# Kernel optimization log

Measured on AMD Instinct MI355X. Metric: run time of the kernel, lower is better.

Reference implementation:

```python
import jax, jax.numpy as jnp
import numpy as np

B, N_VIS, N_HID1, N_HID2 = 1024, 4096, 4096, 4096


def setup_inputs() -> dict:
    key = jax.random.key(0)
    k0, k1, k2, k3 = jax.random.split(key, 4)
    v_data = (jax.random.uniform(k0, (B, N_VIS)) < 0.5).astype(jnp.float32)
    occupant_data = (jax.random.uniform(k1, (B, N_VIS // 2)) < 0.5).astype(jnp.float32)
    bw1 = float(np.sqrt(6.0 / (N_HID1 + N_VIS)))   # xavier_uniform
    bw2 = float(np.sqrt(6.0 / (N_HID1 + N_HID2)))
    W1 = jax.random.uniform(k2, (N_HID1, N_VIS), jnp.float32, -bw1, bw1)
    W2 = jax.random.uniform(k3, (N_HID1, N_HID2), jnp.float32, -bw2, bw2)
    return {
        "v_data": v_data,
        "occupant_data": occupant_data,
        "W1": W1,
        "b_v": jnp.zeros((N_VIS,), jnp.float32),
        "b_h1": jnp.zeros((N_HID1,), jnp.float32),
        "W2": W2,
        "b_h2": jnp.zeros((N_HID2,), jnp.float32),
        "k": 2,
    }


def reference(v_data, occupant_data, W1, b_v, b_h1, W2, b_h2, k):
    key = jax.random.key(42)
    Bn, n_vis = v_data.shape
    n_hid2 = b_h2.shape[0]
    dt = v_data.dtype

    def bern(kk, p):
        return (jax.random.uniform(kk, p.shape, p.dtype) < p).astype(p.dtype)

    # literal torch math (n_hid1 == n_hid2):
    # F.linear(v, W1, b_h1) + F.linear(h2, W2.T) = v@W1.T + b_h1 + h2@W2
    def p_h1(v, h2):
        return jax.nn.sigmoid(v @ W1.T + b_h1 + h2 @ W2)

    def p_h2(h1):  # F.linear(h1, W2, b_h2) = h1@W2.T + b_h2
        return jax.nn.sigmoid(h1 @ W2.T + b_h2)

    def p_v(h1):   # F.linear(h1, W1.T, b_v) = h1@W1 + b_v
        return jax.nn.sigmoid(h1 @ W1 + b_v)

    kpos1, kpos2, kfin, kloop = jax.random.split(key, 4)

    # positive phase (no_grad in torch)
    h2_zeros = jnp.zeros((Bn, n_hid2), dt)
    h1_data = bern(kpos1, jax.lax.stop_gradient(p_h1(v_data, h2_zeros)))
    h2_data = bern(kpos2, jax.lax.stop_gradient(p_h2(h1_data)))

    # negative phase: k Gibbs steps with occupant clamping
    v_neg, h2_neg = v_data, h2_data
    for i in range(k):
        ka, kb, kc = jax.random.split(jax.random.fold_in(kloop, i), 3)
        h1_neg = bern(ka, p_h1(v_neg, h2_neg))
        h2_neg = bern(kb, p_h2(h1_neg))
        pv = p_v(h1_neg)
        sign_s = bern(kc, pv[:, 1::2])
        # occupant_clamp: occupant bits from data, sign bits sampled
        v_neg = jnp.stack([occupant_data, sign_s], axis=-1).reshape(Bn, n_vis)

    h1_neg_final = bern(kfin, jax.lax.stop_gradient(p_h1(v_neg, h2_neg)))

    pos_v_sign = v_data[:, 1::2]
    neg_v_sign = v_neg[:, 1::2]
    invB = 1.0 / Bn

    # mean over batch of outer products == single matmul / B
    dW1_sign = (jnp.einsum('bi,bj->ij', pos_v_sign, h1_data)
                - jnp.einsum('bi,bj->ij', neg_v_sign, h1_neg_final)) * invB
    dW1_full = jnp.zeros_like(W1).at[:, 1::2].set(dW1_sign.T)
    db_v_full = jnp.zeros_like(b_v).at[1::2].set((pos_v_sign - neg_v_sign).mean(0))
    db_h1 = (h1_data - h1_neg_final).mean(0)
    dW2 = (jnp.einsum('bi,bj->ij', h1_data, h2_data)
           - jnp.einsum('bi,bj->ij', h1_neg_final, h2_neg)) * invB
    db_h2 = (h2_data - h2_neg).mean(0)

    eps = jnp.asarray(1e-7, dt)
    sp, st = v_neg[:, 1::2], v_data[:, 1::2]
    loss = -(st * jnp.log(sp + eps) + (1 - st) * jnp.log(1 - sp + eps)).mean()

    # torch sets p.grad = -dX; return loss plus those grads
    return (loss, -dW1_full, -db_v_full, -db_h1, -dW2, -db_h2)
```

## Files before the change

kernel.cpp:

```cpp
#include <hip/hip_runtime.h>
#include <stdint.h>
#include <math.h>

#define B_SZ 1024
#define NV   4096
#define NH   4096
#define NSGN 2048

typedef short bf16x8 __attribute__((ext_vector_type(8)));
typedef short bf16x4 __attribute__((ext_vector_type(4)));
typedef float f32x4  __attribute__((ext_vector_type(4)));
typedef _Float16 f16x8 __attribute__((ext_vector_type(8)));

#define F16_ONE  ((short)0x3C00)
#define F16_NEG1 ((short)0xBC00)

__device__ __forceinline__ short f32_to_f16s(float f)
{
    union { _Float16 h; short s; } u;
    u.h = (_Float16)f;
    return u.s;
}

__host__ __device__ __forceinline__ void tf2x32(uint32_t k0, uint32_t k1,
                                                uint32_t x0, uint32_t x1,
                                                uint32_t& o0, uint32_t& o1)
{
    uint32_t k2 = k0 ^ k1 ^ 0x1BD11BDAu;
#define TFR(r) { x0 += x1; x1 = (x1 << (r)) | (x1 >> (32 - (r))); x1 ^= x0; }
    x0 += k0; x1 += k1;
    TFR(13) TFR(15) TFR(26) TFR(6)
    x0 += k1; x1 += k2 + 1u;
    TFR(17) TFR(29) TFR(16) TFR(24)
    x0 += k2; x1 += k0 + 2u;
    TFR(13) TFR(15) TFR(26) TFR(6)
    x0 += k0; x1 += k1 + 3u;
    TFR(17) TFR(29) TFR(16) TFR(24)
    x0 += k1; x1 += k2 + 4u;
    TFR(13) TFR(15) TFR(26) TFR(6)
    x0 += k2; x1 += k0 + 5u;
#undef TFR
    o0 = x0; o1 = x1;
}

__device__ __forceinline__ float tf_uniform01(uint32_t k0, uint32_t k1, uint32_t idx)
{
    uint32_t a, b;
    tf2x32(k0, k1, 0u, idx, a, b);
    uint32_t bits = a ^ b;
    uint32_t fb = (bits >> 9) | 0x3F800000u;
    return __uint_as_float(fb) - 1.0f;
}

__device__ __forceinline__ float sigmoidf_(float x)
{
    if (x >= 0.0f) { float e = expf(-x); return 1.0f / (1.0f + e); }
    float e = expf(x); return e / (1.0f + e);
}

__device__ __forceinline__ void gl16(const void* g, void* l)
{
    __builtin_amdgcn_global_load_lds((const __attribute__((address_space(1))) void*)g,
                                     (__attribute__((address_space(3))) void*)l, 16, 0, 0);
}

__global__ __launch_bounds__(256) void conv_tr(const float* __restrict__ W,
                                               short* __restrict__ Wf,
                                               short* __restrict__ Wt)
{
    __shared__ short t[64][65];
    const int bx = blockIdx.x * 64;
    const int by = blockIdx.y * 64;
    const int r0 = threadIdx.x >> 4;
    const int c0 = (threadIdx.x & 15) * 4;
#pragma unroll
    for (int i = 0; i < 4; ++i) {
        int row = by + r0 + i * 16;
        f32x4 v = *(const f32x4*)(W + (size_t)row * 4096 + bx + c0);
        short h[4];
#pragma unroll
        for (int j = 0; j < 4; ++j) h[j] = f32_to_f16s(v[j]);
        *(bf16x4*)(Wf + (size_t)row * 4096 + bx + c0) = *(bf16x4*)h;
#pragma unroll
        for (int j = 0; j < 4; ++j) t[c0 + j][r0 + i * 16] = h[j];
    }
    __syncthreads();
#pragma unroll
    for (int i = 0; i < 4; ++i) {
        int orow = r0 + i * 16;
        short o[4] = { t[orow][c0], t[orow][c0 + 1], t[orow][c0 + 2], t[orow][c0 + 3] };
        *(bf16x4*)(Wt + (size_t)(bx + orow) * 4096 + by + c0) = *(bf16x4*)o;
    }
}

__global__ __launch_bounds__(256) void conv_f16(const float* __restrict__ W,
                                                short* __restrict__ Wf)
{
    size_t i = ((size_t)blockIdx.x * 256 + threadIdx.x) * 4;
    f32x4 v = *(const f32x4*)(W + i);
    short h[4];
#pragma unroll
    for (int c = 0; c < 4; ++c) h[c] = f32_to_f16s(v[c]);
    *(bf16x4*)(Wf + i) = *(bf16x4*)h;
}

__global__ __launch_bounds__(256) void conv_trodd(const float* __restrict__ W,
                                                  short* __restrict__ Wt)
{
    __shared__ short t[64][65];
    const int bx = blockIdx.x * 64;
    const int by = blockIdx.y * 64;
    const int r0 = threadIdx.x >> 4;
    const int c0 = (threadIdx.x & 15) * 4;
#pragma unroll
    for (int i = 0; i < 4; ++i) {
        int row = by + r0 + i * 16;
        const float* p = W + (size_t)row * 4096 + 2 * (bx + c0);
        f32x4 a = *(const f32x4*)p;
        f32x4 b = *(const f32x4*)(p + 4);
        t[c0 + 0][r0 + i * 16] = f32_to_f16s(a[1]);
        t[c0 + 1][r0 + i * 16] = f32_to_f16s(a[3]);
        t[c0 + 2][r0 + i * 16] = f32_to_f16s(b[1]);
        t[c0 + 3][r0 + i * 16] = f32_to_f16s(b[3]);
    }
    __syncthreads();
#pragma unroll
    for (int i = 0; i < 4; ++i) {
        int orow = r0 + i * 16;
        short o[4] = { t[orow][c0], t[orow][c0 + 1], t[orow][c0 + 2], t[orow][c0 + 3] };
        *(bf16x4*)(Wt + (size_t)(bx + orow) * 4096 + by + c0) = *(bf16x4*)o;
    }
}

template<int NEG>
__global__ __launch_bounds__(256) void tr16(const short* __restrict__ in,
                                            short* __restrict__ out)
{
    __shared__ short t[64][65];
    const int bx = blockIdx.x * 64;
    const int by = blockIdx.y * 64;
    const int r0 = threadIdx.x >> 4;
    const int c0 = (threadIdx.x & 15) * 4;
#pragma unroll
    for (int i = 0; i < 4; ++i) {
        int row = by + r0 + i * 16;
        bf16x4 v = *(const bf16x4*)(in + (size_t)row * 4096 + bx + c0);
#pragma unroll
        for (int j = 0; j < 4; ++j)
            t[c0 + j][r0 + i * 16] = NEG ? (short)(v[j] ^ (short)0x8000) : v[j];
    }
    __syncthreads();
#pragma unroll
    for (int i = 0; i < 4; ++i) {
        int orow = r0 + i * 16;
        short o[4] = { t[orow][c0], t[orow][c0 + 1], t[orow][c0 + 2], t[orow][c0 + 3] };
        *(bf16x4*)(out + (size_t)(bx + orow) * 1024 + by + c0) = *(bf16x4*)o;
    }
}

__global__ __launch_bounds__(256) void tr_sign(const short* __restrict__ in,
                                               short* __restrict__ out)
{
    __shared__ short t[64][65];
    const int bx = blockIdx.x * 64;
    const int by = blockIdx.y * 64;
    const int r0 = threadIdx.x >> 4;
    const int c0 = (threadIdx.x & 15) * 4;
#pragma unroll
    for (int i = 0; i < 4; ++i) {
        int row = by + r0 + i * 16;
        bf16x8 v = *(const bf16x8*)(in + (size_t)row * 4096 + 2 * (bx + c0));
#pragma unroll
        for (int j = 0; j < 4; ++j) t[c0 + j][r0 + i * 16] = v[2 * j + 1];
    }
    __syncthreads();
#pragma unroll
    for (int i = 0; i < 4; ++i) {
        int orow = r0 + i * 16;
        short o[4] = { t[orow][c0], t[orow][c0 + 1], t[orow][c0 + 2], t[orow][c0 + 3] };
        *(bf16x4*)(out + (size_t)(bx + orow) * 1024 + by + c0) = *(bf16x4*)o;
    }
}

__global__ __launch_bounds__(256) void tr_signf(const float* __restrict__ in,
                                                short* __restrict__ out)
{
    __shared__ short t[64][65];
    const int bx = blockIdx.x * 64;
    const int by = blockIdx.y * 64;
    const int r0 = threadIdx.x >> 4;
    const int c0 = (threadIdx.x & 15) * 4;
#pragma unroll
    for (int i = 0; i < 4; ++i) {
        int row = by + r0 + i * 16;
        const float* p = in + (size_t)row * 4096 + 2 * (bx + c0);
        f32x4 a = *(const f32x4*)p;
        f32x4 b = *(const f32x4*)(p + 4);
        t[c0 + 0][r0 + i * 16] = (a[1] != 0.0f) ? F16_NEG1 : (short)0;
        t[c0 + 1][r0 + i * 16] = (a[3] != 0.0f) ? F16_NEG1 : (short)0;
        t[c0 + 2][r0 + i * 16] = (b[1] != 0.0f) ? F16_NEG1 : (short)0;
        t[c0 + 3][r0 + i * 16] = (b[3] != 0.0f) ? F16_NEG1 : (short)0;
    }
    __syncthreads();
#pragma unroll
    for (int i = 0; i < 4; ++i) {
        int orow = r0 + i * 16;
        short o[4] = { t[orow][c0], t[orow][c0 + 1], t[orow][c0 + 2], t[orow][c0 + 3] };
        *(bf16x4*)(out + (size_t)(bx + orow) * 1024 + by + c0) = *(bf16x4*)o;
    }
}

template<int MODE>
__global__ __launch_bounds__(512, 2) void mm_chunk(
    const short* __restrict__ A0, const short* __restrict__ A1,
    const short* __restrict__ B0, const short* __restrict__ B1,
    short* __restrict__ P)
{
    __shared__ __align__(1024) short As[2][16 * 512];
    __shared__ __align__(1024) short Bs[2][8 * 512];

    const int bid = blockIdx.x;
    const int xcd = bid & 7, slot = bid >> 3;

    int bm, bncol, ck, kbase, NW;
    const short* Ap;
    const short* Bp;
    if (MODE == 2) {
        int slot6 = slot % 6, rest = slot / 6;
        int pn = xcd * 6 + slot6;
        bm = (rest & 3) * 256;
        ck = rest >> 2;
        kbase = ck * 2048;
        Ap = A0;
        Bp = (pn < 32) ? (B0 + (size_t)pn * 128 * 4096)
                       : (B1 + (size_t)(pn - 32) * 128 * 4096);
        bncol = pn * 128;
        NW = 6144;
    } else {
        int pn = xcd * 4 + (slot & 3);
        bm = ((slot >> 2) & 3) * 256;
        ck = slot >> 4;
        if (MODE == 1) {
            if (ck >= 2) { Ap = A1; Bp = B1 + (size_t)pn * 128 * 4096; kbase = (ck - 2) * 2048; }
            else         { Ap = A0; Bp = B0 + (size_t)pn * 128 * 4096; kbase = ck * 2048; }
        } else {
            Ap = A0; Bp = B0 + (size_t)pn * 128 * 4096; kbase = ck * 1024;
        }
        bncol = pn * 128;
        NW = 4096;
    }

    const int NT = (MODE == 0) ? 32 : 64;

    const int tid = threadIdx.x;
    const int wv = tid >> 6, lane = tid & 63;
    const int l15 = lane & 15, l4 = lane >> 4;
    const int fr = l15, fc = l4 * 8;
    const int wm = wv >> 1, wn = wv & 1;

    f32x4 acc[4][4] = {};

    auto stage = [&](int buf, int t) {
        const int kk = kbase + t * 32;
        gl16(Ap + (size_t)(bm + (wv * 2 + 0) * 16 + fr) * 4096 + kk + fc, &As[buf][(wv * 2 + 0) * 512]);
        gl16(Ap + (size_t)(bm + (wv * 2 + 1) * 16 + fr) * 4096 + kk + fc, &As[buf][(wv * 2 + 1) * 512]);
        gl16(Bp + (size_t)(wv * 16 + fr) * 4096 + kk + fc, &Bs[buf][wv * 512]);
    };
    auto compute = [&](int buf) {
        f16x8 xf[4], yf[4];
#pragma unroll
        for (int m = 0; m < 4; ++m)
            xf[m] = *(f16x8*)&As[buf][(wm * 4 + m) * 512 + lane * 8];
#pragma unroll
        for (int n = 0; n < 4; ++n)
            yf[n] = *(f16x8*)&Bs[buf][(wn * 4 + n) * 512 + lane * 8];
#pragma unroll
        for (int m = 0; m < 4; ++m)
#pragma unroll
            for (int n = 0; n < 4; ++n)
                acc[m][n] = __builtin_amdgcn_mfma_f32_16x16x32_f16(xf[m], yf[n], acc[m][n], 0, 0, 0);
    };

    stage(0, 0);
    __syncthreads();
    for (int t = 0; t < NT; ++t) {
        const int cur = t & 1;
        if (t + 1 < NT) stage(cur ^ 1, t + 1);
        compute(cur);
        __syncthreads();
    }

    short* Pc = P + (size_t)ck * 1024 * NW;
#pragma unroll
    for (int m = 0; m < 4; ++m)
#pragma unroll
        for (int n = 0; n < 4; ++n)
#pragma unroll
            for (int r = 0; r < 4; ++r) {
                int row = bm + wm * 64 + m * 16 + l4 * 4 + r;
                int col = bncol + wn * 64 + n * 16 + l15;
                Pc[(size_t)row * NW + col] = f32_to_f16s(acc[m][n][r]);
            }
}

__global__ __launch_bounds__(512, 2) void grad2(
    const short* __restrict__ XnT, const short* __restrict__ YnT,
    const short* __restrict__ XpT, const short* __restrict__ YpT,
    float* __restrict__ Out)
{
    __shared__ __align__(1024) short As[2][16 * 512];
    __shared__ __align__(1024) short Bs[2][8 * 512];

    const int bid = blockIdx.x;
    const int xcd = bid & 7, slot = bid >> 3;
    const int pn = xcd * 4 + (slot & 3);
    const int bm = (slot >> 2) * 256;

    const int tid = threadIdx.x;
    const int wv = tid >> 6, lane = tid & 63;
    const int l15 = lane & 15, l4 = lane >> 4;
    const int fr = l15, fc = l4 * 8;
    const int wm = wv >> 1, wn = wv & 1;

    f32x4 acc[4][4] = {};

    auto stage = [&](int buf, int t) {
        const short* X = (t < 32) ? XnT : XpT;
        const short* Y = (t < 32) ? YnT : YpT;
        const int kk = (t & 31) * 32;
        gl16(X + (size_t)(bm + (wv * 2 + 0) * 16 + fr) * 1024 + kk + fc, &As[buf][(wv * 2 + 0) * 512]);
        gl16(X + (size_t)(bm + (wv * 2 + 1) * 16 + fr) * 1024 + kk + fc, &As[buf][(wv * 2 + 1) * 512]);
        gl16(Y + (size_t)(pn * 128 + wv * 16 + fr) * 1024 + kk + fc, &Bs[buf][wv * 512]);
    };
    auto compute = [&](int buf) {
        f16x8 xf[4], yf[4];
#pragma unroll
        for (int m = 0; m < 4; ++m)
            xf[m] = *(f16x8*)&As[buf][(wm * 4 + m) * 512 + lane * 8];
#pragma unroll
        for (int n = 0; n < 4; ++n)
            yf[n] = *(f16x8*)&Bs[buf][(wn * 4 + n) * 512 + lane * 8];
#pragma unroll
        for (int m = 0; m < 4; ++m)
#pragma unroll
            for (int n = 0; n < 4; ++n)
                acc[m][n] = __builtin_amdgcn_mfma_f32_16x16x32_f16(xf[m], yf[n], acc[m][n], 0, 0, 0);
    };

    stage(0, 0);
    __syncthreads();
    for (int t = 0; t < 64; ++t) {
        const int cur = t & 1;
        if (t + 1 < 64) stage(cur ^ 1, t + 1);
        compute(cur);
        __syncthreads();
    }

    const float invB = 1.0f / 1024.0f;
#pragma unroll
    for (int m = 0; m < 4; ++m)
#pragma unroll
        for (int n = 0; n < 4; ++n)
#pragma unroll
            for (int r = 0; r < 4; ++r) {
                int i_ = bm + wm * 64 + m * 16 + l4 * 4 + r;
                int j_ = pn * 128 + wn * 64 + n * 16 + l15;
                Out[(size_t)i_ * 4096 + j_] = acc[m][n][r] * invB;
            }
}

__global__ __launch_bounds__(256, 4) void grad1(
    const short* __restrict__ XnT, const short* __restrict__ YnT,
    const short* __restrict__ XpT, const short* __restrict__ YpT,
    float* __restrict__ Out)
{
    __shared__ __align__(1024) short As[2][8 * 512];
    __shared__ __align__(1024) short Bs[2][8 * 512];

    const int bid = blockIdx.x;
    const int xcd = bid & 7, slot = bid >> 3;
    const int pn = xcd * 2 + (slot & 1);
    const int bm = (slot >> 1) * 128;

    const int tid = threadIdx.x;
    const int wv = tid >> 6, lane = tid & 63;
    const int l15 = lane & 15, l4 = lane >> 4;
    const int fr = l15, fc = l4 * 8;
    const int wm = wv >> 1, wn = wv & 1;

    f32x4 acc[4][4] = {};

    auto stage = [&](int buf, int t) {
        const short* X = (t < 32) ? XnT : XpT;
        const short* Y = (t < 32) ? YnT : YpT;
        const int kk = (t & 31) * 32;
#pragma unroll
        for (int c = 0; c < 2; ++c) {
            int sub = wv * 2 + c;
            gl16(X + (size_t)(bm + sub * 16 + fr) * 1024 + kk + fc, &As[buf][sub * 512]);
            gl16(Y + (size_t)(pn * 128 + sub * 16 + fr) * 1024 + kk + fc, &Bs[buf][sub * 512]);
        }
    };
    auto compute = [&](int buf) {
        f16x8 xf[4], yf[4];
#pragma unroll
        for (int m = 0; m < 4; ++m)
            xf[m] = *(f16x8*)&As[buf][(wm * 4 + m) * 512 + lane * 8];
#pragma unroll
        for (int n = 0; n < 4; ++n)
            yf[n] = *(f16x8*)&Bs[buf][(wn * 4 + n) * 512 + lane * 8];
#pragma unroll
        for (int m = 0; m < 4; ++m)
#pragma unroll
            for (int n = 0; n < 4; ++n)
                acc[m][n] = __builtin_amdgcn_mfma_f32_16x16x32_f16(xf[m], yf[n], acc[m][n], 0, 0, 0);
    };

    stage(0, 0);
    __syncthreads();
    for (int t = 0; t < 64; ++t) {
        const int cur = t & 1;
        if (t + 1 < 64) stage(cur ^ 1, t + 1);
        compute(cur);
        __syncthreads();
    }

    const float invB = 1.0f / 1024.0f;
#pragma unroll
    for (int m = 0; m < 4; ++m)
#pragma unroll
        for (int n = 0; n < 4; ++n)
#pragma unroll
            for (int r = 0; r < 4; ++r) {
                int i_ = bm + wm * 64 + m * 16 + l4 * 4 + r;
                int j_ = pn * 128 + wn * 64 + n * 16 + l15;
                Out[(size_t)i_ * 4096 + 2 * j_ + 1] = acc[m][n][r] * invB;
                Out[(size_t)i_ * 4096 + 2 * j_]     = 0.0f;
            }
}

template<int EPI, int NC>
__global__ __launch_bounds__(256) void combine_h(
    const short* __restrict__ P, const float* __restrict__ bias,
    short* __restrict__ O0, short* __restrict__ O1,
    uint32_t k0, uint32_t k1)
{
    size_t e0 = ((size_t)blockIdx.x * 256 + threadIdx.x) * 8;
    float s[8] = {};
#pragma unroll
    for (int c = 0; c < NC; ++c) {
        f16x8 v = *(const f16x8*)(P + (size_t)c * 4194304 + e0);
#pragma unroll
        for (int j = 0; j < 8; ++j) s[j] += (float)v[j];
    }
    int col = (int)(e0 & 4095);
    short o[8];
#pragma unroll
    for (int j = 0; j < 8; ++j) {
        float v = s[j] + bias[col + j];
        float pr = sigmoidf_(v);
        float u = tf_uniform01(k0, k1, (uint32_t)(e0 + j));
        o[j] = (u < pr) ? F16_ONE : (short)0;
    }
    *(bf16x8*)&O0[e0] = *(bf16x8*)o;
    if (EPI == 1) *(bf16x8*)&O1[e0] = *(bf16x8*)o;
}

__global__ __launch_bounds__(256) void combine_dual(
    const short* __restrict__ P,
    const float* __restrict__ b_h2, const float* __restrict__ b_v,
    const float* __restrict__ occ,
    short* __restrict__ h2n, short* __restrict__ vneg,
    uint32_t kb0, uint32_t kb1, uint32_t kc0, uint32_t kc1)
{
    int idx = blockIdx.x * 256 + threadIdx.x;
    int row = idx / 768;
    int cl  = (idx - row * 768) * 8;
    float s[8] = {};
#pragma unroll
    for (int c = 0; c < 2; ++c) {
        f16x8 v = *(const f16x8*)(P + (size_t)c * 6291456 + (size_t)row * 6144 + cl);
#pragma unroll
        for (int j = 0; j < 8; ++j) s[j] += (float)v[j];
    }
    if (cl < 4096) {
        short o[8];
#pragma unroll
        for (int j = 0; j < 8; ++j) {
            float v = s[j] + b_h2[cl + j];
            float pr = sigmoidf_(v);
            size_t e = (size_t)row * 4096 + cl + j;
            float u = tf_uniform01(kb0, kb1, (uint32_t)e);
            o[j] = (u < pr) ? F16_ONE : (short)0;
        }
        *(bf16x8*)&h2n[(size_t)row * 4096 + cl] = *(bf16x8*)o;
    } else {
        int s0 = cl - 4096;
        short o[16];
#pragma unroll
        for (int j = 0; j < 8; ++j) {
            int si = s0 + j;
            float v = s[j] + b_v[2 * si + 1];
            float pr = sigmoidf_(v);
            float u = tf_uniform01(kc0, kc1, (uint32_t)(row * 2048 + si));
            o[2 * j]     = (occ[(size_t)row * 2048 + si] != 0.0f) ? F16_ONE : (short)0;
            o[2 * j + 1] = (u < pr) ? F16_ONE : (short)0;
        }
        *(bf16x8*)&vneg[(size_t)row * 4096 + 2 * s0]     = *(bf16x8*)&o[0];
        *(bf16x8*)&vneg[(size_t)row * 4096 + 2 * s0 + 8] = *(bf16x8*)&o[8];
    }
}

__global__ void cvt_kernel(const float* __restrict__ in, short* __restrict__ out, int n)
{
    int e = blockIdx.x * 256 + threadIdx.x;
    if (e < n) out[e] = (in[e] != 0.0f) ? F16_ONE : (short)0;
}

__global__ void dbv_fast(const float* __restrict__ vdata, const short* __restrict__ vneg,
                         float* __restrict__ out)
{
    __shared__ float part[4][64];
    int c = threadIdx.x & 63, rg = threadIdx.x >> 6;
    int s = blockIdx.x * 64 + c;
    float acc = 0.0f;
    for (int b = rg; b < B_SZ; b += 4)
        acc += ((vneg[(size_t)b * NV + 2 * s + 1] != 0) ? 1.0f : 0.0f)
             - vdata[(size_t)b * NV + 2 * s + 1];
    part[rg][c] = acc;
    __syncthreads();
    if (rg == 0) {
        out[2 * s + 1] = (part[0][c] + part[1][c] + part[2][c] + part[3][c]) * (1.0f / 1024.0f);
        out[2 * s] = 0.0f;
    }
}

__global__ void dbh_fast(const short* __restrict__ Xp, const short* __restrict__ Xn,
                         float* __restrict__ out)
{
    __shared__ int part[4][64];
    int c = threadIdx.x & 63, rg = threadIdx.x >> 6;
    int j = blockIdx.x * 64 + c;
    int acc = 0;
    for (int b = rg; b < B_SZ; b += 4)
        acc += (int)(Xn[(size_t)b * NH + j] != 0) - (int)(Xp[(size_t)b * NH + j] != 0);
    part[rg][c] = acc;
    __syncthreads();
    if (rg == 0)
        out[j] = (float)(part[0][c] + part[1][c] + part[2][c] + part[3][c]) * (1.0f / 1024.0f);
}

__global__ void zero_kernel(unsigned* p) { *p = 0u; }

__global__ void loss_count2(const float* __restrict__ vdata,
                            const short* __restrict__ vneg, unsigned* cnt)
{
    __shared__ int part[4];
    int t = blockIdx.x * 256 + threadIdx.x;
    int local = 0;
#pragma unroll
    for (int it = 0; it < 8; ++it) {
        int e = t + it * 262144;
        int b = e >> 11, s = e & 2047;
        float st = vdata[(size_t)b * NV + 2 * s + 1];
        float sp = (vneg[(size_t)b * NV + 2 * s + 1] != 0) ? 1.0f : 0.0f;
        local += (st != sp) ? 1 : 0;
    }
#pragma unroll
    for (int off = 32; off; off >>= 1) local += __shfl_down(local, off, 64);
    if ((threadIdx.x & 63) == 0) part[threadIdx.x >> 6] = local;
    __syncthreads();
    if (threadIdx.x == 0)
        atomicAdd(cnt, (unsigned)(part[0] + part[1] + part[2] + part[3]));
}

__global__ void loss_final_kernel(const unsigned* cnt, float* out, float lp, float lm)
{
    float mis = (float)(*cnt);
    float mat = 2097152.0f - mis;
    out[0] = -((mat * lp + mis * lm) * (1.0f / 2097152.0f));
}

extern "C" void kernel_launch(void* const* d_in, const int* in_sizes, int n_in,
                              void* d_out, int out_size, void* d_ws, size_t ws_size,
                              hipStream_t stream)
{
    (void)in_sizes; (void)n_in; (void)out_size; (void)ws_size;
    const float* v_data = (const float*)d_in[0];
    const float* occ    = (const float*)d_in[1];
    const float* W1     = (const float*)d_in[2];
    const float* b_v    = (const float*)d_in[3];
    const float* b_h1   = (const float*)d_in[4];
    const float* W2     = (const float*)d_in[5];
    const float* b_h2   = (const float*)d_in[6];
    float* out = (float*)d_out;

    char* w = (char*)d_ws;
    short* vneg = (short*)w;
    short* h1d  = vneg + (size_t)B_SZ * NV;
    short* h2d  = h1d  + (size_t)B_SZ * NH;
    short* h1c  = h2d  + (size_t)B_SZ * NH;
    short* h2n  = h1c  + (size_t)B_SZ * NH;
    short* P    = h2n + (size_t)B_SZ * NH;
    unsigned* cnt = (unsigned*)(P + (size_t)20 * 1024 * 1024);

    short* h1cT  = P;
    short* h1dT  = h1cT  + (size_t)4096 * 1024;
    short* h2nT  = h1dT  + (size_t)4096 * 1024;
    short* h2dTn = h2nT  + (size_t)4096 * 1024;
    short* vsT   = h2dTn + (size_t)4096 * 1024;
    short* vdsTn = vsT   + (size_t)2048 * 1024;

    short* W1f  = (short*)(((uintptr_t)(out + 1) + 15) & ~(uintptr_t)15);
    short* W1To = W1f  + (size_t)NH * NV;
    short* W2f  = W1To + (size_t)NSGN * NV;
    short* W2T  = W2f  + (size_t)NH * NH;

    const uint32_t r0 = 0u, r1 = 42u;
    uint32_t kp1a, kp1b, kp2a, kp2b, kfa, kfb, kla, klb;
    tf2x32(r0, r1, 0u, 0u, kp1a, kp1b);
    tf2x32(r0, r1, 0u, 1u, kp2a, kp2b);
    tf2x32(r0, r1, 0u, 2u, kfa, kfb);
    tf2x32(r0, r1, 0u, 3u, kla, klb);
    uint32_t kaA[2], kaB[2], kbA[2], kbB[2], kcA[2], kcB[2];
    for (int i = 0; i < 2; ++i) {
        uint32_t fa, fb;
        tf2x32(kla, klb, 0u, (uint32_t)i, fa, fb);
        tf2x32(fa, fb, 0u, 0u, kaA[i], kaB[i]);
        tf2x32(fa, fb, 0u, 1u, kbA[i], kbB[i]);
        tf2x32(fa, fb, 0u, 2u, kcA[i], kcB[i]);
    }

    const int T = 256;
    const int NELEM = B_SZ * NH;

    conv_f16<<<(NH * NV) / (4 * 256), 256, 0, stream>>>(W1, W1f);
    conv_trodd<<<dim3(32, 64), 256, 0, stream>>>(W1, W1To);
    conv_tr<<<dim3(64, 64), 256, 0, stream>>>(W2, W2f, W2T);

    cvt_kernel<<<NELEM / T, T, 0, stream>>>(v_data, vneg, NELEM);

    mm_chunk<0><<<512, 512, 0, stream>>>(vneg, nullptr, W1f, nullptr, P);
    combine_h<0, 4><<<2048, 256, 0, stream>>>(P, b_h1, h1d, nullptr, kp1a, kp1b);
    mm_chunk<0><<<512, 512, 0, stream>>>(h1d, nullptr, W2f, nullptr, P);
    combine_h<1, 4><<<2048, 256, 0, stream>>>(P, b_h2, h2d, h2n, kp2a, kp2b);

    for (int i = 0; i < 2; ++i) {
        mm_chunk<1><<<512, 512, 0, stream>>>(vneg, h2n, W1f, W2T, P);
        combine_h<0, 4><<<2048, 256, 0, stream>>>(P, b_h1, h1c, nullptr, kaA[i], kaB[i]);
        mm_chunk<2><<<384, 512, 0, stream>>>(h1c, nullptr, W2f, W1To, P);
        combine_dual<<<3072, 256, 0, stream>>>(P, b_h2, b_v, occ, h2n, vneg,
                                               kbA[i], kbB[i], kcA[i], kcB[i]);
    }

    mm_chunk<1><<<512, 512, 0, stream>>>(vneg, h2n, W1f, W2T, P);
    combine_h<0, 4><<<2048, 256, 0, stream>>>(P, b_h1, h1c, nullptr, kfa, kfb);

    float* dW1o  = out + 1;
    float* dbvo  = dW1o + (size_t)NH * NV;
    float* dbh1o = dbvo + NV;
    float* dW2o  = dbh1o + NH;
    float* dbh2o = dW2o + (size_t)NH * NH;

    dim3 gT16(64, 16), gTS(32, 16);
    tr16<0><<<gT16, 256, 0, stream>>>(h1c, h1cT);
    tr16<0><<<gT16, 256, 0, stream>>>(h1d, h1dT);
    tr16<0><<<gT16, 256, 0, stream>>>(h2n, h2nT);
    tr16<1><<<gT16, 256, 0, stream>>>(h2d, h2dTn);
    tr_sign<<<gTS, 256, 0, stream>>>(vneg, vsT);
    tr_signf<<<gTS, 256, 0, stream>>>(v_data, vdsTn);

    grad1<<<512, 256, 0, stream>>>(h1cT, vsT, h1dT, vdsTn, dW1o);
    grad2<<<512, 512, 0, stream>>>(h1cT, h2nT, h1dT, h2dTn, dW2o);

    dbv_fast<<<NSGN / 64, T, 0, stream>>>(v_data, vneg, dbvo);
    dbh_fast<<<NH / 64, T, 0, stream>>>(h1d, h1c, dbh1o);
    dbh_fast<<<NH / 64, T, 0, stream>>>(h2d, h2n, dbh2o);

    zero_kernel<<<1, 1, 0, stream>>>(cnt);
    loss_count2<<<1024, T, 0, stream>>>(v_data, vneg, cnt);
    loss_final_kernel<<<1, 1, 0, stream>>>(cnt, out, logf(1.0f + 1e-7f), logf(1e-7f));
}
```

Measured before the change: 1.183 ms.

## Run gradient outer-product GEMMs in FP8 using binary 0/±1 operands

The transposed binary sample matrices (h1, h2, v sign bits) are now written as 1-byte FP8 values (0, +1, -1) instead of FP16. The grad1/grad2 GEMMs switch to fp8 MFMA, with new LDS staging and fragment offsets for 8-byte operands. Because the operands are exactly 0 or ±1, FP8 represents them losslessly. The aim is to halve transpose and GEMM operand traffic and use the faster FP8 MFMA rate, at the cost of new fragment-layout indexing that must exactly match the fp8 instruction's expected operand layout.

```diff
diff --git a/kernel.cpp b/kernel.cpp
--- a/kernel.cpp
+++ b/kernel.cpp
@@ -11,9 +11,11 @@
 typedef short bf16x4 __attribute__((ext_vector_type(4)));
 typedef float f32x4  __attribute__((ext_vector_type(4)));
 typedef _Float16 f16x8 __attribute__((ext_vector_type(8)));
+typedef unsigned char uchar;
 
 #define F16_ONE  ((short)0x3C00)
-#define F16_NEG1 ((short)0xBC00)
+#define F8_ONE   ((uchar)0x38)
+#define F8_NEG1  ((uchar)0xB8)
 
 __device__ __forceinline__ short f32_to_f16s(float f)
 {
@@ -133,35 +135,36 @@
 }
 
 template<int NEG>
-__global__ __launch_bounds__(256) void tr16(const short* __restrict__ in,
-                                            short* __restrict__ out)
-{
-    __shared__ short t[64][65];
+__global__ __launch_bounds__(256) void tr8(const short* __restrict__ in,
+                                           uchar* __restrict__ out)
+{
+    __shared__ uchar t[64][68];
     const int bx = blockIdx.x * 64;
     const int by = blockIdx.y * 64;
     const int r0 = threadIdx.x >> 4;
     const int c0 = (threadIdx.x & 15) * 4;
+    const uchar ONE = NEG ? F8_NEG1 : F8_ONE;
 #pragma unroll
     for (int i = 0; i < 4; ++i) {
         int row = by + r0 + i * 16;
         bf16x4 v = *(const bf16x4*)(in + (size_t)row * 4096 + bx + c0);
 #pragma unroll
         for (int j = 0; j < 4; ++j)
-            t[c0 + j][r0 + i * 16] = NEG ? (short)(v[j] ^ (short)0x8000) : v[j];
+            t[c0 + j][r0 + i * 16] = (v[j] != 0) ? ONE : (uchar)0;
     }
     __syncthreads();
 #pragma unroll
     for (int i = 0; i < 4; ++i) {
         int orow = r0 + i * 16;
-        short o[4] = { t[orow][c0], t[orow][c0 + 1], t[orow][c0 + 2], t[orow][c0 + 3] };
-        *(bf16x4*)(out + (size_t)(bx + orow) * 1024 + by + c0) = *(bf16x4*)o;
-    }
-}
-
-__global__ __launch_bounds__(256) void tr_sign(const short* __restrict__ in,
-                                               short* __restrict__ out)
-{
-    __shared__ short t[64][65];
+        uchar o[4] = { t[orow][c0], t[orow][c0 + 1], t[orow][c0 + 2], t[orow][c0 + 3] };
+        *(uint32_t*)(out + (size_t)(bx + orow) * 1024 + by + c0) = *(uint32_t*)o;
+    }
+}
+
+__global__ __launch_bounds__(256) void tr_sign8(const short* __restrict__ in,
+                                                uchar* __restrict__ out)
+{
+    __shared__ uchar t[64][68];
     const int bx = blockIdx.x * 64;
     const int by = blockIdx.y * 64;
     const int r0 = threadIdx.x >> 4;
@@ -171,21 +174,22 @@
         int row = by + r0 + i * 16;
         bf16x8 v = *(const bf16x8*)(in + (size_t)row * 4096 + 2 * (bx + c0));
 #pragma unroll
-        for (int j = 0; j < 4; ++j) t[c0 + j][r0 + i * 16] = v[2 * j + 1];
+        for (int j = 0; j < 4; ++j)
+            t[c0 + j][r0 + i * 16] = (v[2 * j + 1] != 0) ? F8_ONE : (uchar)0;
     }
     __syncthreads();
 #pragma unroll
     for (int i = 0; i < 4; ++i) {
         int orow = r0 + i * 16;
-        short o[4] = { t[orow][c0], t[orow][c0 + 1], t[orow][c0 + 2], t[orow][c0 + 3] };
-        *(bf16x4*)(out + (size_t)(bx + orow) * 1024 + by + c0) = *(bf16x4*)o;
-    }
-}
-
-__global__ __launch_bounds__(256) void tr_signf(const float* __restrict__ in,
-                                                short* __restrict__ out)
-{
-    __shared__ short t[64][65];
+        uchar o[4] = { t[orow][c0], t[orow][c0 + 1], t[orow][c0 + 2], t[orow][c0 + 3] };
+        *(uint32_t*)(out + (size_t)(bx + orow) * 1024 + by + c0) = *(uint32_t*)o;
+    }
+}
+
+__global__ __launch_bounds__(256) void tr_signf8(const float* __restrict__ in,
+                                                 uchar* __restrict__ out)
+{
+    __shared__ uchar t[64][68];
     const int bx = blockIdx.x * 64;
     const int by = blockIdx.y * 64;
     const int r0 = threadIdx.x >> 4;
@@ -196,17 +200,17 @@
         const float* p = in + (size_t)row * 4096 + 2 * (bx + c0);
         f32x4 a = *(const f32x4*)p;
         f32x4 b = *(const f32x4*)(p + 4);
-        t[c0 + 0][r0 + i * 16] = (a[1] != 0.0f) ? F16_NEG1 : (short)0;
-        t[c0 + 1][r0 + i * 16] = (a[3] != 0.0f) ? F16_NEG1 : (short)0;
-        t[c0 + 2][r0 + i * 16] = (b[1] != 0.0f) ? F16_NEG1 : (short)0;
-        t[c0 + 3][r0 + i * 16] = (b[3] != 0.0f) ? F16_NEG1 : (short)0;
+        t[c0 + 0][r0 + i * 16] = (a[1] != 0.0f) ? F8_NEG1 : (uchar)0;
+        t[c0 + 1][r0 + i * 16] = (a[3] != 0.0f) ? F8_NEG1 : (uchar)0;
+        t[c0 + 2][r0 + i * 16] = (b[1] != 0.0f) ? F8_NEG1 : (uchar)0;
+        t[c0 + 3][r0 + i * 16] = (b[3] != 0.0f) ? F8_NEG1 : (uchar)0;
     }
     __syncthreads();
 #pragma unroll
     for (int i = 0; i < 4; ++i) {
         int orow = r0 + i * 16;
-        short o[4] = { t[orow][c0], t[orow][c0 + 1], t[orow][c0 + 2], t[orow][c0 + 3] };
-        *(bf16x4*)(out + (size_t)(bx + orow) * 1024 + by + c0) = *(bf16x4*)o;
+        uchar o[4] = { t[orow][c0], t[orow][c0 + 1], t[orow][c0 + 2], t[orow][c0 + 3] };
+        *(uint32_t*)(out + (size_t)(bx + orow) * 1024 + by + c0) = *(uint32_t*)o;
     }
 }
 
@@ -304,12 +308,12 @@
 }
 
 __global__ __launch_bounds__(512, 2) void grad2(
-    const short* __restrict__ XnT, const short* __restrict__ YnT,
-    const short* __restrict__ XpT, const short* __restrict__ YpT,
+    const uchar* __restrict__ XnT, const uchar* __restrict__ YnT,
+    const uchar* __restrict__ XpT, const uchar* __restrict__ YpT,
     float* __restrict__ Out)
 {
-    __shared__ __align__(1024) short As[2][16 * 512];
-    __shared__ __align__(1024) short Bs[2][8 * 512];
+    __shared__ __align__(1024) uchar As[2][16 * 512];
+    __shared__ __align__(1024) uchar Bs[2][8 * 512];
 
     const int bid = blockIdx.x;
     const int xcd = bid & 7, slot = bid >> 3;
@@ -319,32 +323,35 @@
     const int tid = threadIdx.x;
     const int wv = tid >> 6, lane = tid & 63;
     const int l15 = lane & 15, l4 = lane >> 4;
-    const int fr = l15, fc = l4 * 8;
+    const int sl = lane & 31, lh = lane >> 5;
     const int wm = wv >> 1, wn = wv & 1;
+    const int foff = (l4 >> 1) * 256 + l15 * 16 + (l4 & 1) * 8;
 
     f32x4 acc[4][4] = {};
 
     auto stage = [&](int buf, int t) {
-        const short* X = (t < 32) ? XnT : XpT;
-        const short* Y = (t < 32) ? YnT : YpT;
+        const uchar* X = (t < 32) ? XnT : XpT;
+        const uchar* Y = (t < 32) ? YnT : YpT;
         const int kk = (t & 31) * 32;
-        gl16(X + (size_t)(bm + (wv * 2 + 0) * 16 + fr) * 1024 + kk + fc, &As[buf][(wv * 2 + 0) * 512]);
-        gl16(X + (size_t)(bm + (wv * 2 + 1) * 16 + fr) * 1024 + kk + fc, &As[buf][(wv * 2 + 1) * 512]);
-        gl16(Y + (size_t)(pn * 128 + wv * 16 + fr) * 1024 + kk + fc, &Bs[buf][wv * 512]);
+        gl16(X + (size_t)(bm + (2 * wv + lh) * 16 + (sl & 15)) * 1024 + kk + (sl >> 4) * 16,
+             &As[buf][wv * 1024]);
+        if (wv < 4)
+            gl16(Y + (size_t)(pn * 128 + (2 * wv + lh) * 16 + (sl & 15)) * 1024 + kk + (sl >> 4) * 16,
+                 &Bs[buf][wv * 1024]);
     };
     auto compute = [&](int buf) {
-        f16x8 xf[4], yf[4];
+        long xf[4], yf[4];
 #pragma unroll
         for (int m = 0; m < 4; ++m)
-            xf[m] = *(f16x8*)&As[buf][(wm * 4 + m) * 512 + lane * 8];
+            xf[m] = *(long*)&As[buf][(wm * 4 + m) * 512 + foff];
 #pragma unroll
         for (int n = 0; n < 4; ++n)
-            yf[n] = *(f16x8*)&Bs[buf][(wn * 4 + n) * 512 + lane * 8];
+            yf[n] = *(long*)&Bs[buf][(wn * 4 + n) * 512 + foff];
 #pragma unroll
         for (int m = 0; m < 4; ++m)
 #pragma unroll
             for (int n = 0; n < 4; ++n)
-                acc[m][n] = __builtin_amdgcn_mfma_f32_16x16x32_f16(xf[m], yf[n], acc[m][n], 0, 0, 0);
+                acc[m][n] = __builtin_amdgcn_mfma_f32_16x16x32_fp8_fp8(xf[m], yf[n], acc[m][n], 0, 0, 0);
     };
 
     stage(0, 0);
@@ -370,12 +377,12 @@
 }
 
 __global__ __launch_bounds__(256, 4) void grad1(
-    const short* __restrict__ XnT, const short* __restrict__ YnT,
-    const short* __restrict__ XpT, const short* __restrict__ YpT,
+    const uchar* __restrict__ XnT, const uchar* __restrict__ YnT,
+    const uchar* __restrict__ XpT, const uchar* __restrict__ YpT,
     float* __restrict__ Out)
 {
-    __shared__ __align__(1024) short As[2][8 * 512];
-    __shared__ __align__(1024) short Bs[2][8 * 512];
+    __shared__ __align__(1024) uchar As[2][8 * 512];
+    __shared__ __align__(1024) uchar Bs[2][8 * 512];
 
     const int bid = blockIdx.x;
     const int xcd = bid & 7, slot = bid >> 3;
@@ -385,35 +392,34 @@
     const int tid = threadIdx.x;
     const int wv = tid >> 6, lane = tid & 63;
     const int l15 = lane & 15, l4 = lane >> 4;
-    const int fr = l15, fc = l4 * 8;
+    const int sl = lane & 31, lh = lane >> 5;
     const int wm = wv >> 1, wn = wv & 1;
+    const int foff = (l4 >> 1) * 256 + l15 * 16 + (l4 & 1) * 8;
 
     f32x4 acc[4][4] = {};
 
     auto stage = [&](int buf, int t) {
-        const short* X = (t < 32) ? XnT : XpT;
-        const short* Y = (t < 32) ? YnT : YpT;
+        const uchar* X = (t < 32) ? XnT : XpT;
+        const uchar* Y = (t < 32) ? YnT : YpT;
         const int kk = (t & 31) * 32;
-#pragma unroll
-        for (int c = 0; c < 2; ++c) {
-            int sub = wv * 2 + c;
-            gl16(X + (size_t)(bm + sub * 16 + fr) * 1024 + kk + fc, &As[buf][sub * 512]);
-            gl16(Y + (size_t)(pn * 128 + sub * 16 + fr) * 1024 + kk + fc, &Bs[buf][sub * 512]);
-        }
+        gl16(X + (size_t)(bm + (2 * wv + lh) * 16 + (sl & 15)) * 1024 + kk + (sl >> 4) * 16,
+             &As[buf][wv * 1024]);
+        gl16(Y + (size_t)(pn * 128 + (2 * wv + lh) * 16 + (sl & 15)) * 1024 + kk + (sl >> 4) * 16,
+             &Bs[buf][wv * 1024]);
     };
     auto compute = [&](int buf) {
-        f16x8 xf[4], yf[4];
+        long xf[4], yf[4];
 #pragma unroll
         for (int m = 0; m < 4; ++m)
-            xf[m] = *(f16x8*)&As[buf][(wm * 4 + m) * 512 + lane * 8];
+            xf[m] = *(long*)&As[buf][(wm * 4 + m) * 512 + foff];
 #pragma unroll
         for (int n = 0; n < 4; ++n)
-            yf[n] = *(f16x8*)&Bs[buf][(wn * 4 + n) * 512 + lane * 8];
+            yf[n] = *(long*)&Bs[buf][(wn * 4 + n) * 512 + foff];
 #pragma unroll
         for (int m = 0; m < 4; ++m)
 #pragma unroll
             for (int n = 0; n < 4; ++n)
-                acc[m][n] = __builtin_amdgcn_mfma_f32_16x16x32_f16(xf[m], yf[n], acc[m][n], 0, 0, 0);
+                acc[m][n] = __builtin_amdgcn_mfma_f32_16x16x32_fp8_fp8(xf[m], yf[n], acc[m][n], 0, 0, 0);
     };
 
     stage(0, 0);
@@ -604,12 +610,12 @@
     short* P    = h2n + (size_t)B_SZ * NH;
     unsigned* cnt = (unsigned*)(P + (size_t)20 * 1024 * 1024);
 
-    short* h1cT  = P;
-    short* h1dT  = h1cT  + (size_t)4096 * 1024;
-    short* h2nT  = h1dT  + (size_t)4096 * 1024;
-    short* h2dTn = h2nT  + (size_t)4096 * 1024;
-    short* vsT   = h2dTn + (size_t)4096 * 1024;
-    short* vdsTn = vsT   + (size_t)2048 * 1024;
+    uchar* h1cT8  = (uchar*)P;
+    uchar* h1dT8  = h1cT8  + (size_t)4096 * 1024;
+    uchar* h2nT8  = h1dT8  + (size_t)4096 * 1024;
+    uchar* h2dT8n = h2nT8  + (size_t)4096 * 1024;
+    uchar* vsT8   = h2dT8n + (size_t)4096 * 1024;
+    uchar* vdsT8n = vsT8   + (size_t)2048 * 1024;
 
     short* W1f  = (short*)(((uintptr_t)(out + 1) + 15) & ~(uintptr_t)15);
     short* W1To = W1f  + (size_t)NH * NV;
@@ -663,15 +669,15 @@
     float* dbh2o = dW2o + (size_t)NH * NH;
 
     dim3 gT16(64, 16), gTS(32, 16);
-    tr16<0><<<gT16, 256, 0, stream>>>(h1c, h1cT);
-    tr16<0><<<gT16, 256, 0, stream>>>(h1d, h1dT);
-    tr16<0><<<gT16, 256, 0, stream>>>(h2n, h2nT);
-    tr16<1><<<gT16, 256, 0, stream>>>(h2d, h2dTn);
-    tr_sign<<<gTS, 256, 0, stream>>>(vneg, vsT);
-    tr_signf<<<gTS, 256, 0, stream>>>(v_data, vdsTn);
-
-    grad1<<<512, 256, 0, stream>>>(h1cT, vsT, h1dT, vdsTn, dW1o);
-    grad2<<<512, 512, 0, stream>>>(h1cT, h2nT, h1dT, h2dTn, dW2o);
+    tr8<0><<<gT16, 256, 0, stream>>>(h1c, h1cT8);
+    tr8<0><<<gT16, 256, 0, stream>>>(h1d, h1dT8);
+    tr8<0><<<gT16, 256, 0, stream>>>(h2n, h2nT8);
+    tr8<1><<<gT16, 256, 0, stream>>>(h2d, h2dT8n);
+    tr_sign8<<<gTS, 256, 0, stream>>>(vneg, vsT8);
+    tr_signf8<<<gTS, 256, 0, stream>>>(v_data, vdsT8n);
+
+    grad1<<<512, 256, 0, stream>>>(h1cT8, vsT8, h1dT8, vdsT8n, dW1o);
+    grad2<<<512, 512, 0, stream>>>(h1cT8, h2nT8, h1dT8, h2dT8n, dW2o);
 
     dbv_fast<<<NSGN / 64, T, 0, stream>>>(v_data, vneg, dbvo);
     dbh_fast<<<NH / 64, T, 0, stream>>>(h1d, h1c, dbh1o);
```

Result: faster. 1.129 ms (-4.6%).
